# Optimization experiments

Measured on AMD Instinct MI355X. Metric: run time of the kernel, lower is better.

## Reference

```python
import jax, jax.numpy as jnp
import numpy as np

N, E, D = 40000, 640000, 128
BN_EPS = 1e-5  # torch BatchNorm1d default eps


def setup_inputs() -> dict:
    key = jax.random.key(0)
    ks = jax.random.split(key, 4)
    x = jax.random.normal(ks[0], (N, D), dtype=jnp.float32)
    edge_index = jax.random.randint(ks[1], (2, E), 0, N, dtype=jnp.int32)
    # Learned params: GIN message MLP = single Linear(D, D); outer BatchNorm1d affine; learnable eps.
    W = jax.random.normal(ks[2], (D, D), dtype=jnp.float32) / np.sqrt(D).astype(np.float32)
    b = jnp.zeros((D,), jnp.float32)
    gamma = jnp.ones((D,), jnp.float32)
    beta = jnp.zeros((D,), jnp.float32)
    gin_eps = jnp.zeros((1,), jnp.float32)  # train_eps=True, init 0.0
    return {"x": x, "edge_index": edge_index, "W": W, "b": b,
            "gamma": gamma, "beta": beta, "gin_eps": gin_eps}


def reference(x, edge_index, W, b, gamma, beta, gin_eps):
    src, dst = edge_index[0], edge_index[1]
    # GIN aggregation: out[i] = (1+eps)*x[i] + sum_{(j->i) in E} x[j]
    agg = jax.ops.segment_sum(x[src], dst, num_segments=x.shape[0])  # [N, D]
    h = (1.0 + gin_eps[0]) * x + agg
    # message MLP: single Linear
    h = h @ W.T + b
    # BatchNorm1d over node dim (training-mode batch stats, biased variance)
    mean = jnp.mean(h, axis=0)
    var = jnp.mean(jnp.square(h - mean), axis=0)
    h = gamma * (h - mean) * jax.lax.rsqrt(var + BN_EPS) + beta
    # activation (dropout p=0 is identity) + residual
    h = jax.nn.relu(h)
    return h + x
```

## Files before the change

kernel.cpp:

```cpp
#include <hip/hip_runtime.h>
#include <hip/hip_bf16.h>

#define D 128
#define DH 64
#define CAP 56
#define SC 8
#define CS 16

typedef unsigned int uint32;
typedef __attribute__((ext_vector_type(8))) short bf16x8;
typedef __attribute__((ext_vector_type(4))) float f32x4;

__device__ __forceinline__ float bflo(uint32 u) { return __uint_as_float(u << 16); }
__device__ __forceinline__ float bfhi(uint32 u) { return __uint_as_float(u & 0xffff0000u); }
__device__ __forceinline__ unsigned short f2bf(float f) {
    uint32 u = __float_as_uint(f);
    return (unsigned short)((u + 0x7FFFu + ((u >> 16) & 1u)) >> 16);
}

__global__ __launch_bounds__(256) void fillcompress_kernel(
    const int* __restrict__ src, const int* __restrict__ dst,
    int* __restrict__ cnt, int* __restrict__ esrc,
    const float4* __restrict__ x4, uint2* __restrict__ xh2,
    const float4* __restrict__ W4, uint2* __restrict__ W16,
    float* __restrict__ statp, int E, int N)
{
    const int gtid  = blockIdx.x * 256 + threadIdx.x;
    const int gsize = gridDim.x * 256;
    const uint32 sent = (uint32)cnt[(long)N * CS];

    if (gtid < SC * 256) statp[gtid] = 0.0f;

    for (int e = gtid; e < E; e += gsize) {
        int d = dst[e];
        int s = src[e];
        if ((unsigned)d < (unsigned)N) {
            uint32 old = (uint32)atomicAdd(&cnt[(long)d * CS], 1);
            uint32 p = old - sent;
            if (p < (uint32)CAP) {
                esrc[(long)d * CAP + p] = min(max(s, 0), N - 1);
            }
        }
    }

    const long total = (long)N * 32;
    for (long idx = gtid; idx < total; idx += gsize) {
        float4 v = x4[idx];
        uint2 o;
        o.x = (uint32)f2bf(v.x) | ((uint32)f2bf(v.y) << 16);
        o.y = (uint32)f2bf(v.z) | ((uint32)f2bf(v.w) << 16);
        xh2[idx] = o;
    }

    for (int idx = gtid; idx < (D * D) / 4; idx += gsize) {
        float4 v = W4[idx];
        uint2 o;
        o.x = (uint32)f2bf(v.x) | ((uint32)f2bf(v.y) << 16);
        o.y = (uint32)f2bf(v.z) | ((uint32)f2bf(v.w) << 16);
        W16[idx] = o;
    }
}

#define ROWL(nm, k, jj) \
    uint4 nm; { int j_ = ((k) < deg) ? (jj) : 0; nm = xh4[j_ * 16 + l16]; }

#define BMASK(P, B) \
    if ((B) + 0 >= deg) { (P##0).x = 0u; (P##0).y = 0u; (P##0).z = 0u; (P##0).w = 0u; } \
    if ((B) + 1 >= deg) { (P##1).x = 0u; (P##1).y = 0u; (P##1).z = 0u; (P##1).w = 0u; } \
    if ((B) + 2 >= deg) { (P##2).x = 0u; (P##2).y = 0u; (P##2).z = 0u; (P##2).w = 0u; } \
    if ((B) + 3 >= deg) { (P##3).x = 0u; (P##3).y = 0u; (P##3).z = 0u; (P##3).w = 0u; } \
    if ((B) + 4 >= deg) { (P##4).x = 0u; (P##4).y = 0u; (P##4).z = 0u; (P##4).w = 0u; } \
    if ((B) + 5 >= deg) { (P##5).x = 0u; (P##5).y = 0u; (P##5).z = 0u; (P##5).w = 0u; } \
    if ((B) + 6 >= deg) { (P##6).x = 0u; (P##6).y = 0u; (P##6).z = 0u; (P##6).w = 0u; } \
    if ((B) + 7 >= deg) { (P##7).x = 0u; (P##7).y = 0u; (P##7).z = 0u; (P##7).w = 0u; }

#define ACC8(P) \
    a0 += (bflo((P##0).x)+bflo((P##1).x)) + (bflo((P##2).x)+bflo((P##3).x)) \
        + (bflo((P##4).x)+bflo((P##5).x)) + (bflo((P##6).x)+bflo((P##7).x)); \
    a1 += (bfhi((P##0).x)+bfhi((P##1).x)) + (bfhi((P##2).x)+bfhi((P##3).x)) \
        + (bfhi((P##4).x)+bfhi((P##5).x)) + (bfhi((P##6).x)+bfhi((P##7).x)); \
    a2 += (bflo((P##0).y)+bflo((P##1).y)) + (bflo((P##2).y)+bflo((P##3).y)) \
        + (bflo((P##4).y)+bflo((P##5).y)) + (bflo((P##6).y)+bflo((P##7).y)); \
    a3 += (bfhi((P##0).y)+bfhi((P##1).y)) + (bfhi((P##2).y)+bfhi((P##3).y)) \
        + (bfhi((P##4).y)+bfhi((P##5).y)) + (bfhi((P##6).y)+bfhi((P##7).y)); \
    a4 += (bflo((P##0).z)+bflo((P##1).z)) + (bflo((P##2).z)+bflo((P##3).z)) \
        + (bflo((P##4).z)+bflo((P##5).z)) + (bflo((P##6).z)+bflo((P##7).z)); \
    a5 += (bfhi((P##0).z)+bfhi((P##1).z)) + (bfhi((P##2).z)+bfhi((P##3).z)) \
        + (bfhi((P##4).z)+bfhi((P##5).z)) + (bfhi((P##6).z)+bfhi((P##7).z)); \
    a6 += (bflo((P##0).w)+bflo((P##1).w)) + (bflo((P##2).w)+bflo((P##3).w)) \
        + (bflo((P##4).w)+bflo((P##5).w)) + (bflo((P##6).w)+bflo((P##7).w)); \
    a7 += (bfhi((P##0).w)+bfhi((P##1).w)) + (bfhi((P##2).w)+bfhi((P##3).w)) \
        + (bfhi((P##4).w)+bfhi((P##5).w)) + (bfhi((P##6).w)+bfhi((P##7).w));

__global__ __launch_bounds__(256, 4) void gathergemm_kernel(
    const uint4* __restrict__ xh4,
    const int* __restrict__ cnt, const int* __restrict__ esrc,
    const unsigned short* __restrict__ W16, const float* __restrict__ bb,
    const float* __restrict__ geps, float* __restrict__ hlin,
    float* __restrict__ statp, int N)
{
    __shared__ __align__(16) unsigned short hl[16][136];
    __shared__ float bias_s[D];

    const int tid = threadIdx.x;
    if (tid < D) bias_s[tid] = bb[tid];
    const float eps1 = 1.0f + geps[0];
    const uint32 sent = (uint32)cnt[(long)N * CS];
    const int row0 = blockIdx.x * 16;

    const int grp = tid >> 4;
    const int l16 = tid & 15;
    {
        const int node = row0 + grp;
        float a0=0.f,a1=0.f,a2=0.f,a3=0.f,a4=0.f,a5=0.f,a6=0.f,a7=0.f;
        int deg = 0; long base = 0;
        int4 ja0 = {0,0,0,0}, jb0 = {0,0,0,0}, ja1 = {0,0,0,0}, jb1 = {0,0,0,0},
             ja2 = {0,0,0,0}, jb2 = {0,0,0,0}, ja3 = {0,0,0,0}, jb3 = {0,0,0,0};
        if (node < N) {
            deg  = min((int)((uint32)cnt[(long)node * CS] - sent), CAP);
            base = (long)node * CAP;
            const int4* jp = (const int4*)(esrc + base);
            ja0 = jp[0]; jb0 = jp[1]; ja1 = jp[2]; jb1 = jp[3];
            ja2 = jp[4]; jb2 = jp[5]; ja3 = jp[6]; jb3 = jp[7];
            uint4 sx = xh4[(long)node * 16 + l16];
            a0 = bflo(sx.x) * eps1; a1 = bfhi(sx.x) * eps1;
            a2 = bflo(sx.y) * eps1; a3 = bfhi(sx.y) * eps1;
            a4 = bflo(sx.z) * eps1; a5 = bfhi(sx.z) * eps1;
            a6 = bflo(sx.w) * eps1; a7 = bfhi(sx.w) * eps1;
        }
        ROWL(u00,  0, ja0.x) ROWL(u01,  1, ja0.y) ROWL(u02,  2, ja0.z) ROWL(u03,  3, ja0.w)
        ROWL(u04,  4, jb0.x) ROWL(u05,  5, jb0.y) ROWL(u06,  6, jb0.z) ROWL(u07,  7, jb0.w)
        ROWL(u10,  8, ja1.x) ROWL(u11,  9, ja1.y) ROWL(u12, 10, ja1.z) ROWL(u13, 11, ja1.w)
        ROWL(u14, 12, jb1.x) ROWL(u15, 13, jb1.y) ROWL(u16, 14, jb1.z) ROWL(u17, 15, jb1.w)
        ROWL(u20, 16, ja2.x) ROWL(u21, 17, ja2.y) ROWL(u22, 18, ja2.z) ROWL(u23, 19, ja2.w)
        ROWL(u24, 20, jb2.x) ROWL(u25, 21, jb2.y) ROWL(u26, 22, jb2.z) ROWL(u27, 23, jb2.w)
        BMASK(u0, 0)
        ACC8(u0)
        ROWL(u30, 24, ja3.x) ROWL(u31, 25, ja3.y) ROWL(u32, 26, ja3.z) ROWL(u33, 27, ja3.w)
        ROWL(u34, 28, jb3.x) ROWL(u35, 29, jb3.y) ROWL(u36, 30, jb3.z) ROWL(u37, 31, jb3.w)
        BMASK(u1, 8)
        ACC8(u1)
        BMASK(u2, 16)
        ACC8(u2)
        BMASK(u3, 24)
        ACC8(u3)
        for (int e = 32; e < deg; ++e) {
            int j = esrc[base + e];
            uint4 u = xh4[j * 16 + l16];
            a0 += bflo(u.x); a1 += bfhi(u.x);
            a2 += bflo(u.y); a3 += bfhi(u.y);
            a4 += bflo(u.z); a5 += bfhi(u.z);
            a6 += bflo(u.w); a7 += bfhi(u.w);
        }
        uint4 o;
        o.x = (uint32)f2bf(a0) | ((uint32)f2bf(a1) << 16);
        o.y = (uint32)f2bf(a2) | ((uint32)f2bf(a3) << 16);
        o.z = (uint32)f2bf(a4) | ((uint32)f2bf(a5) << 16);
        o.w = (uint32)f2bf(a6) | ((uint32)f2bf(a7) << 16);
        *(uint4*)&hl[grp][l16 * 8] = o;
    }
    __syncthreads();

    const int wave = tid >> 6;
    const int l64  = tid & 63;
    const int m    = l64 & 15;
    const int quad = l64 >> 4;

    f32x4 acc0 = (f32x4){0.f, 0.f, 0.f, 0.f};
    f32x4 acc1 = (f32x4){0.f, 0.f, 0.f, 0.f};
    const int n0 = (2 * wave) * 16 + m;
    const int n1 = n0 + 16;
    #pragma unroll
    for (int ks = 0; ks < 4; ++ks) {
        bf16x8 afrag = *(const bf16x8*)&hl[m][ks * 32 + quad * 8];
        bf16x8 b0 = *(const bf16x8*)(W16 + ((long)n0 * D + ks * 32 + quad * 8));
        bf16x8 b1 = *(const bf16x8*)(W16 + ((long)n1 * D + ks * 32 + quad * 8));
        acc0 = __builtin_amdgcn_mfma_f32_16x16x32_bf16(afrag, b0, acc0, 0, 0, 0);
        acc1 = __builtin_amdgcn_mfma_f32_16x16x32_bf16(afrag, b1, acc1, 0, 0, 0);
    }

    float* sp = statp + (blockIdx.x & (SC - 1)) * 256;
    #pragma unroll
    for (int t = 0; t < 2; ++t) {
        const int col = t ? n1 : n0;
        const float bias = bias_s[col];
        float ps = 0.f, pq = 0.f;
        #pragma unroll
        for (int r = 0; r < 4; ++r) {
            int gr = row0 + quad * 4 + r;
            float v = (t ? acc1[r] : acc0[r]) + bias;
            if (gr < N) {
                hlin[(long)gr * D + col] = v;
                ps += v;
                pq = fmaf(v, v, pq);
            }
        }
        ps += __shfl_xor(ps, 16); ps += __shfl_xor(ps, 32);
        pq += __shfl_xor(pq, 16); pq += __shfl_xor(pq, 32);
        if (quad == 0) {
            unsafeAtomicAdd(&sp[col],       ps);
            unsafeAtomicAdd(&sp[128 + col], pq);
        }
    }
}

__global__ __launch_bounds__(256) void out_kernel(
    const float2* hlin2, const float2* __restrict__ x2,
    const float* __restrict__ statp, const float* __restrict__ gamma,
    const float* __restrict__ beta, float invN, float2* dout, long total)
{
    __shared__ float ginv[D], sh[D];
    if (threadIdx.x < D) {
        int j = threadIdx.x;
        float s = 0.f, q = 0.f;
        #pragma unroll
        for (int cp = 0; cp < SC; ++cp) {
            s += statp[cp * 256 + j];
            q += statp[cp * 256 + 128 + j];
        }
        float mean = s * invN;
        float var  = q * invN - mean * mean;
        float gv   = gamma[j] * rsqrtf(var + 1e-5f);
        ginv[j] = gv;
        sh[j]   = beta[j] - mean * gv;
    }
    __syncthreads();
    const long stride = (long)gridDim.x * 256;
    for (long t = (long)blockIdx.x * 256 + threadIdx.x; t < total; t += stride) {
        int f = (int)(t & 63);
        float2 hv = hlin2[t];
        float2 xv = x2[t];
        float v0 = fmaf(hv.x, ginv[2 * f],     sh[2 * f]);
        float v1 = fmaf(hv.y, ginv[2 * f + 1], sh[2 * f + 1]);
        v0 = fmaxf(v0, 0.0f) + xv.x;
        v1 = fmaxf(v1, 0.0f) + xv.y;
        dout[t] = make_float2(v0, v1);
    }
}

static inline size_t align16(size_t v) { return (v + 15) & ~(size_t)15; }

extern "C" void kernel_launch(void* const* d_in, const int* in_sizes, int n_in,
                              void* d_out, int out_size, void* d_ws, size_t ws_size,
                              hipStream_t stream)
{
    const float* x     = (const float*)d_in[0];
    const int*   ei    = (const int*)d_in[1];
    const float* W     = (const float*)d_in[2];
    const float* b     = (const float*)d_in[3];
    const float* gamma = (const float*)d_in[4];
    const float* beta  = (const float*)d_in[5];
    const float* geps  = (const float*)d_in[6];

    const int N = in_sizes[0] / D;
    const int E = in_sizes[1] / 2;
    const int* src = ei;
    const int* dst = ei + E;

    char* ws = (char*)d_ws;
    size_t off = 0;
    float* statp = (float*)(ws + off); off += align16((size_t)SC * 256 * 4);
    off = (off + 63) & ~(size_t)63;
    int*   cnt   = (int*)  (ws + off); off += align16((size_t)(N + 1) * CS * 4);
    uint2* xh2   = (uint2*)(ws + off); off += (size_t)N * 32 * 8;
    int*   esrc  = (int*)  (ws + off); off += align16((size_t)N * CAP * 4);
    uint2* W16   = (uint2*)(ws + off); off += (size_t)D * D * 2;

    fillcompress_kernel<<<(E + 255) / 256, 256, 0, stream>>>(
        src, dst, cnt, esrc, (const float4*)x, xh2, (const float4*)W, W16,
        statp, E, N);

    const int mtiles = (N + 15) / 16;
    gathergemm_kernel<<<mtiles, 256, 0, stream>>>(
        (const uint4*)xh2, cnt, esrc,
        (const unsigned short*)W16, b, geps, (float*)d_out, statp, N);

    long ototal = (long)N * DH;
    int oblocks = (int)((ototal + 255) / 256);
    if (oblocks > 2048) oblocks = 2048;
    out_kernel<<<oblocks, 256, 0, stream>>>(
        (const float2*)d_out, (const float2*)x, statp, gamma, beta,
        1.0f / (float)N, (float2*)d_out, ototal);
}
```

Baseline: 157.1 us.

## Store pre-BN linear output as bf16 and overlap edge atomics with conversion

The gather-GEMM kernel now writes its pre-BatchNorm linear output as bf16 into a workspace buffer instead of fp32 into the output, and the output kernel reads that packed bf16. This halves the intermediate write and read traffic, at the cost of bf16 rounding before normalization; the BN statistics are still accumulated from fp32 values. The fill kernel also issues each thread's first edge atomic before the x/W bf16 conversion loops and consumes the returned slot afterward, so atomic latency is meant to overlap with the conversion work.

```diff
diff --git a/kernel.cpp b/kernel.cpp
--- a/kernel.cpp
+++ b/kernel.cpp
@@ -2,7 +2,6 @@
 #include <hip/hip_bf16.h>
 
 #define D 128
-#define DH 64
 #define CAP 56
 #define SC 8
 #define CS 16
@@ -31,15 +30,13 @@
 
     if (gtid < SC * 256) statp[gtid] = 0.0f;
 
-    for (int e = gtid; e < E; e += gsize) {
-        int d = dst[e];
-        int s = src[e];
+    int d = 0, s = 0; uint32 old = 0; bool act = false;
+    if (gtid < E) {
+        d = dst[gtid];
+        s = src[gtid];
         if ((unsigned)d < (unsigned)N) {
-            uint32 old = (uint32)atomicAdd(&cnt[(long)d * CS], 1);
-            uint32 p = old - sent;
-            if (p < (uint32)CAP) {
-                esrc[(long)d * CAP + p] = min(max(s, 0), N - 1);
-            }
+            old = (uint32)atomicAdd(&cnt[(long)d * CS], 1);
+            act = true;
         }
     }
 
@@ -51,13 +48,30 @@
         o.y = (uint32)f2bf(v.z) | ((uint32)f2bf(v.w) << 16);
         xh2[idx] = o;
     }
-
     for (int idx = gtid; idx < (D * D) / 4; idx += gsize) {
         float4 v = W4[idx];
         uint2 o;
         o.x = (uint32)f2bf(v.x) | ((uint32)f2bf(v.y) << 16);
         o.y = (uint32)f2bf(v.z) | ((uint32)f2bf(v.w) << 16);
         W16[idx] = o;
+    }
+
+    if (act) {
+        uint32 p = old - sent;
+        if (p < (uint32)CAP) {
+            esrc[(long)d * CAP + p] = min(max(s, 0), N - 1);
+        }
+    }
+    for (int e = gtid + gsize; e < E; e += gsize) {
+        int dd = dst[e];
+        int ss = src[e];
+        if ((unsigned)dd < (unsigned)N) {
+            uint32 o2 = (uint32)atomicAdd(&cnt[(long)dd * CS], 1);
+            uint32 p = o2 - sent;
+            if (p < (uint32)CAP) {
+                esrc[(long)dd * CAP + p] = min(max(ss, 0), N - 1);
+            }
+        }
     }
 }
 
@@ -96,7 +110,7 @@
     const uint4* __restrict__ xh4,
     const int* __restrict__ cnt, const int* __restrict__ esrc,
     const unsigned short* __restrict__ W16, const float* __restrict__ bb,
-    const float* __restrict__ geps, float* __restrict__ hlin,
+    const float* __restrict__ geps, unsigned short* __restrict__ hlin16,
     float* __restrict__ statp, int N)
 {
     __shared__ __align__(16) unsigned short hl[16][136];
@@ -190,7 +204,7 @@
             int gr = row0 + quad * 4 + r;
             float v = (t ? acc1[r] : acc0[r]) + bias;
             if (gr < N) {
-                hlin[(long)gr * D + col] = v;
+                hlin16[(long)gr * D + col] = f2bf(v);
                 ps += v;
                 pq = fmaf(v, v, pq);
             }
@@ -205,9 +219,10 @@
 }
 
 __global__ __launch_bounds__(256) void out_kernel(
-    const float2* hlin2, const float2* __restrict__ x2,
+    const uint32* __restrict__ h32, const float2* __restrict__ x2,
     const float* __restrict__ statp, const float* __restrict__ gamma,
-    const float* __restrict__ beta, float invN, float2* dout, long total)
+    const float* __restrict__ beta, float invN, float2* __restrict__ dout,
+    long total)
 {
     __shared__ float ginv[D], sh[D];
     if (threadIdx.x < D) {
@@ -228,10 +243,10 @@
     const long stride = (long)gridDim.x * 256;
     for (long t = (long)blockIdx.x * 256 + threadIdx.x; t < total; t += stride) {
         int f = (int)(t & 63);
-        float2 hv = hlin2[t];
+        uint32 hv = h32[t];
         float2 xv = x2[t];
-        float v0 = fmaf(hv.x, ginv[2 * f],     sh[2 * f]);
-        float v1 = fmaf(hv.y, ginv[2 * f + 1], sh[2 * f + 1]);
+        float v0 = fmaf(bflo(hv), ginv[2 * f],     sh[2 * f]);
+        float v1 = fmaf(bfhi(hv), ginv[2 * f + 1], sh[2 * f + 1]);
         v0 = fmaxf(v0, 0.0f) + xv.x;
         v1 = fmaxf(v1, 0.0f) + xv.y;
         dout[t] = make_float2(v0, v1);
@@ -265,6 +280,7 @@
     uint2* xh2   = (uint2*)(ws + off); off += (size_t)N * 32 * 8;
     int*   esrc  = (int*)  (ws + off); off += align16((size_t)N * CAP * 4);
     uint2* W16   = (uint2*)(ws + off); off += (size_t)D * D * 2;
+    unsigned short* hlin16 = (unsigned short*)(ws + off); off += (size_t)N * D * 2;
 
     fillcompress_kernel<<<(E + 255) / 256, 256, 0, stream>>>(
         src, dst, cnt, esrc, (const float4*)x, xh2, (const float4*)W, W16,
@@ -273,12 +289,12 @@
     const int mtiles = (N + 15) / 16;
     gathergemm_kernel<<<mtiles, 256, 0, stream>>>(
         (const uint4*)xh2, cnt, esrc,
-        (const unsigned short*)W16, b, geps, (float*)d_out, statp, N);
-
-    long ototal = (long)N * DH;
+        (const unsigned short*)W16, b, geps, hlin16, statp, N);
+
+    long ototal = (long)N * 64;
     int oblocks = (int)((ototal + 255) / 256);
     if (oblocks > 2048) oblocks = 2048;
     out_kernel<<<oblocks, 256, 0, stream>>>(
-        (const float2*)d_out, (const float2*)x, statp, gamma, beta,
+        (const uint32*)hlin16, (const float2*)x, statp, gamma, beta,
         1.0f / (float)N, (float2*)d_out, ototal);
 }
```

Measured after the change: 155.3 us. No clear change (-1.2%).

## Store linear output in bf16, read bf16 residual, split scatter and convert kernels

Applied to the files above, without the earlier changes.

The GEMM stage now writes its pre-BatchNorm activations as bf16 into a workspace buffer instead of fp32 into the output, and the final normalize kernel reads those bf16 activations plus the bf16 copy of x for the residual instead of fp32 x. This is meant to halve the intermediate write/read traffic and the residual read in the memory-bound epilogue. The fused scatter+convert kernel is also split into two launches, with the conversion using a fixed grid of 2048 blocks. The cost is an extra kernel launch and lower precision, since both the residual and the stored activations are rounded to bf16, which adds output error.

```diff
diff --git a/kernel.cpp b/kernel.cpp
--- a/kernel.cpp
+++ b/kernel.cpp
@@ -2,7 +2,6 @@
 #include <hip/hip_bf16.h>
 
 #define D 128
-#define DH 64
 #define CAP 56
 #define SC 8
 #define CS 16
@@ -18,11 +17,9 @@
     return (unsigned short)((u + 0x7FFFu + ((u >> 16) & 1u)) >> 16);
 }
 
-__global__ __launch_bounds__(256) void fillcompress_kernel(
+__global__ __launch_bounds__(256) void scatter_kernel(
     const int* __restrict__ src, const int* __restrict__ dst,
     int* __restrict__ cnt, int* __restrict__ esrc,
-    const float4* __restrict__ x4, uint2* __restrict__ xh2,
-    const float4* __restrict__ W4, uint2* __restrict__ W16,
     float* __restrict__ statp, int E, int N)
 {
     const int gtid  = blockIdx.x * 256 + threadIdx.x;
@@ -42,6 +39,14 @@
             }
         }
     }
+}
+
+__global__ __launch_bounds__(256) void convert_kernel(
+    const float4* __restrict__ x4, uint2* __restrict__ xh2,
+    const float4* __restrict__ W4, uint2* __restrict__ W16, int N)
+{
+    const int gtid  = blockIdx.x * 256 + threadIdx.x;
+    const int gsize = gridDim.x * 256;
 
     const long total = (long)N * 32;
     for (long idx = gtid; idx < total; idx += gsize) {
@@ -51,7 +56,6 @@
         o.y = (uint32)f2bf(v.z) | ((uint32)f2bf(v.w) << 16);
         xh2[idx] = o;
     }
-
     for (int idx = gtid; idx < (D * D) / 4; idx += gsize) {
         float4 v = W4[idx];
         uint2 o;
@@ -96,7 +100,7 @@
     const uint4* __restrict__ xh4,
     const int* __restrict__ cnt, const int* __restrict__ esrc,
     const unsigned short* __restrict__ W16, const float* __restrict__ bb,
-    const float* __restrict__ geps, float* __restrict__ hlin,
+    const float* __restrict__ geps, unsigned short* __restrict__ hlin16,
     float* __restrict__ statp, int N)
 {
     __shared__ __align__(16) unsigned short hl[16][136];
@@ -190,7 +194,7 @@
             int gr = row0 + quad * 4 + r;
             float v = (t ? acc1[r] : acc0[r]) + bias;
             if (gr < N) {
-                hlin[(long)gr * D + col] = v;
+                hlin16[(long)gr * D + col] = f2bf(v);
                 ps += v;
                 pq = fmaf(v, v, pq);
             }
@@ -205,9 +209,10 @@
 }
 
 __global__ __launch_bounds__(256) void out_kernel(
-    const float2* hlin2, const float2* __restrict__ x2,
+    const uint32* __restrict__ h32, const uint32* __restrict__ xh32,
     const float* __restrict__ statp, const float* __restrict__ gamma,
-    const float* __restrict__ beta, float invN, float2* dout, long total)
+    const float* __restrict__ beta, float invN, float2* __restrict__ dout,
+    long total)
 {
     __shared__ float ginv[D], sh[D];
     if (threadIdx.x < D) {
@@ -228,12 +233,12 @@
     const long stride = (long)gridDim.x * 256;
     for (long t = (long)blockIdx.x * 256 + threadIdx.x; t < total; t += stride) {
         int f = (int)(t & 63);
-        float2 hv = hlin2[t];
-        float2 xv = x2[t];
-        float v0 = fmaf(hv.x, ginv[2 * f],     sh[2 * f]);
-        float v1 = fmaf(hv.y, ginv[2 * f + 1], sh[2 * f + 1]);
-        v0 = fmaxf(v0, 0.0f) + xv.x;
-        v1 = fmaxf(v1, 0.0f) + xv.y;
+        uint32 hv = h32[t];
+        uint32 xv = xh32[t];
+        float v0 = fmaf(bflo(hv), ginv[2 * f],     sh[2 * f]);
+        float v1 = fmaf(bfhi(hv), ginv[2 * f + 1], sh[2 * f + 1]);
+        v0 = fmaxf(v0, 0.0f) + bflo(xv);
+        v1 = fmaxf(v1, 0.0f) + bfhi(xv);
         dout[t] = make_float2(v0, v1);
     }
 }
@@ -265,20 +270,23 @@
     uint2* xh2   = (uint2*)(ws + off); off += (size_t)N * 32 * 8;
     int*   esrc  = (int*)  (ws + off); off += align16((size_t)N * CAP * 4);
     uint2* W16   = (uint2*)(ws + off); off += (size_t)D * D * 2;
-
-    fillcompress_kernel<<<(E + 255) / 256, 256, 0, stream>>>(
-        src, dst, cnt, esrc, (const float4*)x, xh2, (const float4*)W, W16,
-        statp, E, N);
+    unsigned short* hlin16 = (unsigned short*)(ws + off); off += (size_t)N * D * 2;
+
+    scatter_kernel<<<(E + 255) / 256, 256, 0, stream>>>(
+        src, dst, cnt, esrc, statp, E, N);
+
+    convert_kernel<<<2048, 256, 0, stream>>>(
+        (const float4*)x, xh2, (const float4*)W, W16, N);
 
     const int mtiles = (N + 15) / 16;
     gathergemm_kernel<<<mtiles, 256, 0, stream>>>(
         (const uint4*)xh2, cnt, esrc,
-        (const unsigned short*)W16, b, geps, (float*)d_out, statp, N);
-
-    long ototal = (long)N * DH;
+        (const unsigned short*)W16, b, geps, hlin16, statp, N);
+
+    long ototal = (long)N * 64;
     int oblocks = (int)((ototal + 255) / 256);
     if (oblocks > 2048) oblocks = 2048;
     out_kernel<<<oblocks, 256, 0, stream>>>(
-        (const float2*)d_out, (const float2*)x, statp, gamma, beta,
+        (const uint32*)hlin16, (const uint32*)xh2, statp, gamma, beta,
         1.0f / (float)N, (float2*)d_out, ototal);
 }
```

Measured after the change: 156.4 us. Within noise of the previous version (-0.5%).
